# Performance work log

Hardware: AMD Instinct MI355X
Metric: run time of the kernel (lower is better)

## Reference

```python
import jax, jax.numpy as jnp
import numpy as np

L, N, C, OPL = 20, 512, 10, 13        # levels, nodes/level, conditions/node, condition op length
HID, MID = 512, 256                   # hidden_dim, hid_dim
OP_DIM, EX_DIM, SAMP_DIM = 15, 108, 1000
EPS = 1e-5


def _lstm_cell(x, h, c, wih, whh, bih, bhh):
    gates = x @ wih.T + h @ whh.T + bih + bhh
    i, f, g, o = jnp.split(gates, 4, axis=-1)  # torch gate order i,f,g,o
    c = jax.nn.sigmoid(f) * c + jax.nn.sigmoid(i) * jnp.tanh(g)
    h = jax.nn.sigmoid(o) * jnp.tanh(c)
    return h, c


def _batchnorm(x, g, b):  # training-mode BatchNorm1d (biased batch stats)
    m = x.mean(0)
    v = x.var(0)
    return (x - m) / jnp.sqrt(v + EPS) * g + b


def setup_inputs() -> dict:
    key = jax.random.key(0)
    ks = iter(jax.random.split(key, 48))
    rn = lambda shp, s=1.0: jax.random.normal(next(ks), shp, jnp.float32) * s
    ru = lambda shp: jax.random.uniform(next(ks), shp, jnp.float32)
    w = lambda shp: rn(shp, 0.05)
    inp = {
        'operators': ru((L, N, OP_DIM)),
        'extra_infos': rn((L, N, EX_DIM)),
        'condition1s': rn((L, N, C, OPL)),
        'condition2s': rn((L, N, C, OPL)),
        'samples': ru((L, N, SAMP_DIM)),
        'condition_masks': jnp.ones((L, N, 1), jnp.float32),
        'mapping': jax.random.randint(next(ks), (L, 2, N), 0, N + 1),
        # lstm1 (condition encoder)
        'w_ih1': w((4 * HID, OPL)), 'w_hh1': w((4 * HID, HID)),
        'b_ih1': w((4 * HID,)), 'b_hh1': w((4 * HID,)),
        # mlps feeding the tree lstm
        'sample_w': w((MID, SAMP_DIM)), 'sample_b': w((MID,)),
        'cond_w': w((MID, HID)), 'cond_b': w((MID,)),
        'bn1_g': jnp.ones((MID,), jnp.float32), 'bn1_b': jnp.zeros((MID,), jnp.float32),
        # lstm2 (tree aggregation)
        'w_ih2': w((4 * HID, OP_DIM + EX_DIM + 2 * MID)), 'w_hh2': w((4 * HID, HID)),
        'b_ih2': w((4 * HID,)), 'b_hh2': w((4 * HID,)),
        'bn2_g': jnp.ones((HID,), jnp.float32), 'bn2_b': jnp.zeros((HID,), jnp.float32),
        # task heads
        't1_w2': w((MID, HID)), 't1_b2': w((MID,)),
        't2_w2': w((MID, HID)), 't2_b2': w((MID,)),
        'bn3_g': jnp.ones((MID,), jnp.float32), 'bn3_b': jnp.zeros((MID,), jnp.float32),
        't1_w3': w((MID, MID)), 't1_b3': w((MID,)),
        't2_w3': w((MID, MID)), 't2_b3': w((MID,)),
        't1_ow': w((1, MID)), 't1_ob': w((1,)),
        't2_ow': w((1, MID)), 't2_ob': w((1,)),
    }
    return inp


def reference(operators, extra_infos, condition1s, condition2s, samples, condition_masks, mapping,
              w_ih1, w_hh1, b_ih1, b_hh1, sample_w, sample_b, cond_w, cond_b, bn1_g, bn1_b,
              w_ih2, w_hh2, b_ih2, b_hh2, bn2_g, bn2_b,
              t1_w2, t1_b2, t2_w2, t2_b2, bn3_g, bn3_b,
              t1_w3, t1_b3, t2_w3, t2_b3, t1_ow, t1_ob, t2_ow, t2_ob):
    Lv, Np = operators.shape[0], operators.shape[1]
    mapping = mapping.astype(jnp.int32)

    # --- condition encoder: lstm1 over each node's predicate sequence ---
    x = condition1s.reshape(Lv * Np, C, OPL)
    h0 = jnp.zeros((Lv * Np, HID), operators.dtype)

    def step1(carry, xt):
        h, c = carry
        h, c = _lstm_cell(xt, h, c, w_ih1, w_hh1, b_ih1, b_hh1)
        return (h, c), None

    (h_last, _), _ = jax.lax.scan(step1, (h0, h0), jnp.swapaxes(x, 0, 1))
    cond = _batchnorm(jax.nn.relu(h_last @ cond_w.T + cond_b), bn1_g, bn1_b)
    cond = cond.reshape(Lv, Np, MID)

    samp = jax.nn.relu(samples @ sample_w.T + sample_b) * condition_masks
    feats = jnp.concatenate([operators, extra_infos, cond, samp], axis=2)  # [L, N, 123+2*MID]

    # --- bottom level: lstm2 single step from zero state ---
    z0 = jnp.zeros((Np, HID), feats.dtype)
    hid, cid = _lstm_cell(feats[Lv - 1], z0, z0, w_ih2, w_hh2, b_ih2, b_hh2)

    # --- bottom-up tree aggregation: gather children states, average, lstm2 step ---
    def level_step(carry, inputs):
        hid, cid = carry
        x_lvl, mapp = inputs  # x_lvl [N, F], mapp [2, N], index 0 == pad (no child)
        pad = jnp.zeros((1, HID), hid.dtype)
        nh = jnp.concatenate([pad, hid], axis=0)  # [N+1, H]
        nc = jnp.concatenate([pad, cid], axis=0)
        h = (nh[mapp[0]] + nh[mapp[1]]) * 0.5
        c = (nc[mapp[0]] + nc[mapp[1]]) * 0.5
        hid, cid = _lstm_cell(x_lvl, h, c, w_ih2, w_hh2, b_ih2, b_hh2)
        return (hid, cid), None

    xs = (feats[Lv - 2::-1], mapping[Lv - 2::-1])
    (hid, cid), _ = jax.lax.scan(level_step, (hid, cid), xs)

    # --- heads (batch_size == Np: all level-0 nodes active for these inputs) ---
    z = _batchnorm(hid, bn2_g, bn2_b)
    t1 = _batchnorm(jax.nn.relu(z @ t1_w2.T + t1_b2), bn3_g, bn3_b)
    t1 = jax.nn.sigmoid(jax.nn.relu(t1 @ t1_w3.T + t1_b3) @ t1_ow.T + t1_ob)
    t2 = _batchnorm(jax.nn.relu(z @ t2_w2.T + t2_b2), bn3_g, bn3_b)
    t2 = jax.nn.sigmoid(jax.nn.relu(t2 @ t2_w3.T + t2_b3) @ t2_ow.T + t2_ob)
    return t1, t2
```

## Files before the change

kernel.cpp:

```cpp
#include <hip/hip_runtime.h>
#include <hip/hip_bf16.h>


typedef __bf16 bf16x8 __attribute__((ext_vector_type(8)));
typedef float f32x4 __attribute__((ext_vector_type(4)));

#define MROWS 10240
#define LDH1  552
#define L1_ROWS 48
#define L1_BLOCKS 214

#define PF_BIAS1   0
#define PF_BIAS2   2048
#define PF_CONDB   4096
#define PF_SAMPB   4352
#define PF_BCAT2   4608
#define PF_B3CAT   5120
#define PF_BN1G    5632
#define PF_BN1B    5888
#define PF_BN2G    6144
#define PF_BN2B    6656
#define PF_BN3G    7168
#define PF_BN3B    7424
#define PF_OW      7680
#define PF_OB      8192
#define PF_TOTAL   8194

__device__ __forceinline__ float fsig(float x) {
  return __builtin_amdgcn_rcpf(1.0f + __expf(-x));
}
__device__ __forceinline__ float ftanh(float x) {
  return fmaf(2.0f, __builtin_amdgcn_rcpf(1.0f + __expf(-2.0f * x)), -1.0f);
}
__device__ __forceinline__ bf16x8 bzero8() {
  bf16x8 z;
#pragma unroll
  for (int i = 0; i < 8; ++i) z[i] = (__bf16)0.0f;
  return z;
}
__device__ __forceinline__ float ld_in(const void* p, long i, int bf) {
  return bf ? (float)((const __bf16*)p)[i] : ((const float*)p)[i];
}

__global__ void detect_kernel(const unsigned* __restrict__ masks, int* __restrict__ flag) {
  if (blockIdx.x == 0 && threadIdx.x == 0)
    *flag = (masks[0] == 0x3F803F80u) ? 1 : 0;
}

__global__ void prep_kernel(const int* __restrict__ flagp,
    const void* w_ih1, const void* w_hh1, const void* b_ih1, const void* b_hh1,
    const void* w_ih2, const void* w_hh2, const void* b_ih2, const void* b_hh2,
    const void* t1_w2, const void* t2_w2, const void* t1_b2, const void* t2_b2,
    const void* cond_w, const void* cond_b, const void* sample_w, const void* sample_b,
    const void* bn1_g, const void* bn1_b, const void* bn2_g, const void* bn2_b,
    const void* bn3_g, const void* bn3_b,
    const void* t1_w3, const void* t1_b3, const void* t2_w3, const void* t2_b3,
    const void* t1_ow, const void* t1_ob, const void* t2_ow, const void* t2_ob,
    const void* masks,
    __bf16* __restrict__ w1s, __bf16* __restrict__ w2s,
    __bf16* __restrict__ wcat2, __bf16* __restrict__ cond_w_bf,
    __bf16* __restrict__ sample_w_bf, __bf16* __restrict__ w3cat_bf,
    float* __restrict__ mask_f, float* __restrict__ pf)
{
  const int bf = *flagp;
  const int S1 = 2048 * 544;
  const int S2 = 2048 * 1152;
  const int S3 = 512 * 512;
  const int S4 = 256 * 512;
  const int S5 = 256 * 1000;
  const int S6 = 512 * 256;
  const int S7 = 10240;
  const int total = S1 + S2 + S3 + S4 + S5 + S6 + S7 + PF_TOTAL;
  for (int idx = blockIdx.x * blockDim.x + threadIdx.x; idx < total;
       idx += gridDim.x * blockDim.x) {
    int i = idx;
    if (i < S1) {
      int e = i & 7, l = (i >> 3) & 63, g = (i >> 9) & 3;
      int grp = i >> 11;
      int kk = grp % 17, cgt = grp / 17;
      int colq = l & 15, quad = l >> 4;
      int row = g * 512 + cgt * 16 + colq;
      int k = kk * 32 + quad * 8 + e;
      float v = (k < 512) ? ld_in(w_hh1, (long)row * 512 + k, bf)
              : (k < 525) ? ld_in(w_ih1, (long)row * 13 + (k - 512), bf) : 0.0f;
      w1s[i] = (__bf16)v;
      continue;
    }
    i -= S1;
    if (i < S2) {
      int e = i & 7, l = (i >> 3) & 63, g = (i >> 9) & 3;
      int grp = i >> 11;
      int kk = grp % 36, jt = grp / 36;
      int colq = l & 15, quad = l >> 4;
      int row = g * 512 + jt * 16 + colq;
      int k = kk * 32 + quad * 8 + e;
      float v = (k < 635) ? ld_in(w_ih2, (long)row * 635 + k, bf)
              : (k < 640) ? 0.0f : ld_in(w_hh2, (long)row * 512 + (k - 640), bf);
      w2s[i] = (__bf16)v;
      continue;
    }
    i -= S2;
    if (i < S3) {
      int r = i >> 9, k = i & 511;
      wcat2[i] = (__bf16)((r < 256) ? ld_in(t1_w2, r * 512 + k, bf)
                                    : ld_in(t2_w2, (r - 256) * 512 + k, bf));
      continue;
    }
    i -= S3;
    if (i < S4) { cond_w_bf[i] = (__bf16)ld_in(cond_w, i, bf); continue; }
    i -= S4;
    if (i < S5) { sample_w_bf[i] = (__bf16)ld_in(sample_w, i, bf); continue; }
    i -= S5;
    if (i < S6) {
      int r = i >> 8, k = i & 255;
      w3cat_bf[i] = (__bf16)((r < 256) ? ld_in(t1_w3, r * 256 + k, bf)
                                       : ld_in(t2_w3, (r - 256) * 256 + k, bf));
      continue;
    }
    i -= S6;
    if (i < S7) { mask_f[i] = ld_in(masks, i, bf); continue; }
    i -= S7;
    {
      int j = i;
      float v;
      if      (j < 2048) v = ld_in(b_ih1, j, bf) + ld_in(b_hh1, j, bf);
      else if (j < 4096) v = ld_in(b_ih2, j - 2048, bf) + ld_in(b_hh2, j - 2048, bf);
      else if (j < 4352) v = ld_in(cond_b, j - 4096, bf);
      else if (j < 4608) v = ld_in(sample_b, j - 4352, bf);
      else if (j < 5120) { int k = j - 4608; v = (k < 256) ? ld_in(t1_b2, k, bf) : ld_in(t2_b2, k - 256, bf); }
      else if (j < 5632) { int k = j - 5120; v = (k < 256) ? ld_in(t1_b3, k, bf) : ld_in(t2_b3, k - 256, bf); }
      else if (j < 5888) v = ld_in(bn1_g, j - 5632, bf);
      else if (j < 6144) v = ld_in(bn1_b, j - 5888, bf);
      else if (j < 6656) v = ld_in(bn2_g, j - 6144, bf);
      else if (j < 7168) v = ld_in(bn2_b, j - 6656, bf);
      else if (j < 7424) v = ld_in(bn3_g, j - 7168, bf);
      else if (j < 7680) v = ld_in(bn3_b, j - 7424, bf);
      else if (j < 8192) { int k = j - 7680; v = (k < 256) ? ld_in(t1_ow, k, bf) : ld_in(t2_ow, k - 256, bf); }
      else v = (j == 8192) ? ld_in(t1_ob, 0, bf) : ld_in(t2_ob, 0, bf);
      pf[j] = v;
    }
  }
}

__global__ void conv_samples_kernel(const int* __restrict__ flagp,
                                    const void* __restrict__ samples,
                                    __bf16* __restrict__ dst)
{
  const int bf = *flagp;
  if (bf) return;
  for (long i = blockIdx.x * blockDim.x + threadIdx.x; i < 10240000L;
       i += (long)gridDim.x * blockDim.x)
    dst[i] = (__bf16)ld_in(samples, i, bf);
}

__global__ void featcopy_kernel(const int* __restrict__ flagp,
                                const void* __restrict__ ops,
                                const void* __restrict__ extra,
                                __bf16* __restrict__ Astage)
{
  const int bf = *flagp;
  int idx = blockIdx.x * blockDim.x + threadIdx.x;
  int m = idx >> 7, c = idx & 127;
  float v; int col;
  if (c < 15)       { v = ld_in(ops, (long)m * 15 + c, bf);            col = c; }
  else if (c < 123) { v = ld_in(extra, (long)m * 108 + (c - 15), bf);  col = c; }
  else              { v = 0.0f;                                        col = 512 + c; }
  Astage[(size_t)m * 640 + col] = (__bf16)v;
}

__global__ __launch_bounds__(1024, 4) void lstm1_kernel(
    const int* __restrict__ flagp,
    const void* __restrict__ cond1,
    const __bf16* __restrict__ w1s,
    const float*  __restrict__ bias,
    __bf16* __restrict__ h_out)
{
  __shared__ __attribute__((aligned(16))) __bf16 hbuf[2][L1_ROWS * LDH1];
  const int bf   = *flagp;
  const int tid  = threadIdx.x;
  const int wave = tid >> 6;
  const int lane = tid & 63;
  const int colq = lane & 15;
  const int quad = lane >> 4;
  const int r0   = blockIdx.x * L1_ROWS;

  {
    bf16x8 z8 = bzero8();
    for (int i = tid * 8; i < 2 * L1_ROWS * LDH1; i += 1024 * 8)
      *(bf16x8*)&hbuf[0][i] = z8;
  }
  __syncthreads();
  if (tid < L1_ROWS * 8) {
    int row = tid >> 3, jj = tid & 7;
    int gr = r0 + row;
    if (gr < MROWS) {
      long base = (long)gr * 130;
      hbuf[0][row * LDH1 + 512 + jj] = (__bf16)ld_in(cond1, base + jj, bf);
      if (jj < 5) hbuf[0][row * LDH1 + 520 + jj] = (__bf16)ld_in(cond1, base + 8 + jj, bf);
    }
  }
  __syncthreads();

  float c_reg[2][3][4];
#pragma unroll
  for (int a = 0; a < 2; ++a)
#pragma unroll
    for (int b = 0; b < 3; ++b)
#pragma unroll
      for (int r = 0; r < 4; ++r) c_reg[a][b][r] = 0.0f;

  const int jbase = wave * 32;

  float bI[2], bF[2], bG[2], bO[2];
#pragma unroll
  for (int cg = 0; cg < 2; ++cg) {
    const int j = jbase + cg * 16 + colq;
    bI[cg] = bias[j];
    bF[cg] = bias[512 + j];
    bG[cg] = bias[1024 + j];
    bO[cg] = bias[1536 + j];
  }

#pragma unroll 1
  for (int t = 0; t < 10; ++t) {
    const __bf16* hcur = hbuf[t & 1];
    __bf16* hnxt = hbuf[(t + 1) & 1];
#pragma unroll
    for (int cg = 0; cg < 2; ++cg) {
      const int jc = jbase + cg * 16;
      f32x4 acc[3][4];
#pragma unroll
      for (int a = 0; a < 3; ++a)
#pragma unroll
        for (int g = 0; g < 4; ++g)
#pragma unroll
          for (int r = 0; r < 4; ++r) acc[a][g][r] = 0.0f;

      const __bf16* wp = w1s + ((size_t)(wave * 2 + cg) * 17 * 4 * 512) + (lane << 3);
#pragma unroll 1
      for (int kk = 0; kk < 17; ++kk) {
        const int kof = (kk << 5) + (quad << 3);
        bf16x8 af[3];
#pragma unroll
        for (int rt = 0; rt < 3; ++rt)
          af[rt] = *(const bf16x8*)&hcur[(rt * 16 + colq) * LDH1 + kof];
        bf16x8 bfr[4];
#pragma unroll
        for (int g = 0; g < 4; ++g)
          bfr[g] = *(const bf16x8*)&wp[(kk * 4 + g) << 9];
#pragma unroll
        for (int g = 0; g < 4; ++g)
#pragma unroll
          for (int rt = 0; rt < 3; ++rt)
            acc[rt][g] = __builtin_amdgcn_mfma_f32_16x16x32_bf16(af[rt], bfr[g], acc[rt][g], 0, 0, 0);
      }
#pragma unroll
      for (int rt = 0; rt < 3; ++rt)
#pragma unroll
        for (int r = 0; r < 4; ++r) {
          float c = fsig(acc[rt][1][r] + bF[cg]) * c_reg[cg][rt][r]
                  + fsig(acc[rt][0][r] + bI[cg]) * ftanh(acc[rt][2][r] + bG[cg]);
          c_reg[cg][rt][r] = c;
          float h = fsig(acc[rt][3][r] + bO[cg]) * ftanh(c);
          hnxt[(rt * 16 + quad * 4 + r) * LDH1 + jc + colq] = (__bf16)h;
        }
    }
    if (t < 9 && tid < L1_ROWS * 8) {
      int row = tid >> 3, jj = tid & 7;
      int gr = r0 + row;
      if (gr < MROWS) {
        long base = ((long)gr * 10 + (t + 1)) * 13;
        hnxt[row * LDH1 + 512 + jj] = (__bf16)ld_in(cond1, base + jj, bf);
        if (jj < 5) hnxt[row * LDH1 + 520 + jj] = (__bf16)ld_in(cond1, base + 8 + jj, bf);
      }
    }
    __syncthreads();
  }

  for (int i = tid; i < L1_ROWS * 64; i += 1024) {
    int row = i >> 6;
    int cb  = (i & 63) << 3;
    *(bf16x8*)&h_out[(size_t)(r0 + row) * 512 + cb] = *(const bf16x8*)&hbuf[0][row * LDH1 + cb];
  }
}

template<int ACT, int OUTBF, int MASKED>
__global__ __launch_bounds__(256, 4) void gemm_kernel(
    const __bf16* __restrict__ A, int lda,
    const __bf16* __restrict__ W, int ldw,
    const float* __restrict__ bias,
    float* __restrict__ outf, __bf16* __restrict__ outb, int ldc,
    const float* __restrict__ mask, int K)
{
  const int tid  = threadIdx.x;
  const int wave = tid >> 6;
  const int lane = tid & 63;
  const int colq = lane & 15;
  const int quad = lane >> 4;
  const int m0 = blockIdx.y * 64 + (wave >> 1) * 32;
  const int n0 = blockIdx.x * 64 + (wave & 1) * 32;

  f32x4 acc[2][2];
#pragma unroll
  for (int a = 0; a < 2; ++a)
#pragma unroll
    for (int b = 0; b < 2; ++b)
#pragma unroll
      for (int r = 0; r < 4; ++r) acc[a][b][r] = 0.0f;

  const int nk = (K + 31) >> 5;
  for (int kk = 0; kk < nk; ++kk) {
    const int kof = (kk << 5) + (quad << 3);
    bf16x8 a0, a1, b0, b1;
    if (kof < K) {
      a0 = *(const bf16x8*)&A[(size_t)(m0 + colq) * lda + kof];
      a1 = *(const bf16x8*)&A[(size_t)(m0 + 16 + colq) * lda + kof];
      b0 = *(const bf16x8*)&W[(size_t)(n0 + colq) * ldw + kof];
      b1 = *(const bf16x8*)&W[(size_t)(n0 + 16 + colq) * ldw + kof];
    } else {
      a0 = bzero8(); a1 = a0; b0 = a0; b1 = a0;
    }
    acc[0][0] = __builtin_amdgcn_mfma_f32_16x16x32_bf16(a0, b0, acc[0][0], 0, 0, 0);
    acc[0][1] = __builtin_amdgcn_mfma_f32_16x16x32_bf16(a0, b1, acc[0][1], 0, 0, 0);
    acc[1][0] = __builtin_amdgcn_mfma_f32_16x16x32_bf16(a1, b0, acc[1][0], 0, 0, 0);
    acc[1][1] = __builtin_amdgcn_mfma_f32_16x16x32_bf16(a1, b1, acc[1][1], 0, 0, 0);
  }
#pragma unroll
  for (int ai = 0; ai < 2; ++ai)
#pragma unroll
    for (int bi = 0; bi < 2; ++bi) {
      const int col = n0 + bi * 16 + colq;
      const float bv = bias[col];
#pragma unroll
      for (int r = 0; r < 4; ++r) {
        const int row = m0 + ai * 16 + quad * 4 + r;
        float v = acc[ai][bi][r] + bv;
        if (ACT) v = fmaxf(v, 0.0f);
        if (MASKED) v *= mask[row];
        if (OUTBF) outb[(size_t)row * ldc + col] = (__bf16)v;
        else       outf[(size_t)row * ldc + col] = v;
      }
    }
}

__global__ __launch_bounds__(256, 4) void sampgemm_kernel(
    const int* __restrict__ flagp,
    const void* __restrict__ samples_raw,
    const __bf16* __restrict__ samp_bf,
    const __bf16* __restrict__ W,
    const float* __restrict__ bias,
    __bf16* __restrict__ outb,
    const float* __restrict__ mask)
{
  const __bf16* A = (*flagp) ? (const __bf16*)samples_raw : samp_bf;
  const int tid  = threadIdx.x;
  const int wave = tid >> 6;
  const int lane = tid & 63;
  const int colq = lane & 15;
  const int quad = lane >> 4;
  const int m0 = blockIdx.y * 64 + (wave >> 1) * 32;
  const int n0 = blockIdx.x * 64 + (wave & 1) * 32;
  const int K = 1000;

  f32x4 acc[2][2];
#pragma unroll
  for (int a = 0; a < 2; ++a)
#pragma unroll
    for (int b = 0; b < 2; ++b)
#pragma unroll
      for (int r = 0; r < 4; ++r) acc[a][b][r] = 0.0f;

  for (int kk = 0; kk < 32; ++kk) {
    const int kof = (kk << 5) + (quad << 3);
    bf16x8 a0, a1, b0, b1;
    if (kof < K) {
      a0 = *(const bf16x8*)&A[(size_t)(m0 + colq) * 1000 + kof];
      a1 = *(const bf16x8*)&A[(size_t)(m0 + 16 + colq) * 1000 + kof];
      b0 = *(const bf16x8*)&W[(size_t)(n0 + colq) * 1000 + kof];
      b1 = *(const bf16x8*)&W[(size_t)(n0 + 16 + colq) * 1000 + kof];
    } else {
      a0 = bzero8(); a1 = a0; b0 = a0; b1 = a0;
    }
    acc[0][0] = __builtin_amdgcn_mfma_f32_16x16x32_bf16(a0, b0, acc[0][0], 0, 0, 0);
    acc[0][1] = __builtin_amdgcn_mfma_f32_16x16x32_bf16(a0, b1, acc[0][1], 0, 0, 0);
    acc[1][0] = __builtin_amdgcn_mfma_f32_16x16x32_bf16(a1, b0, acc[1][0], 0, 0, 0);
    acc[1][1] = __builtin_amdgcn_mfma_f32_16x16x32_bf16(a1, b1, acc[1][1], 0, 0, 0);
  }
#pragma unroll
  for (int ai = 0; ai < 2; ++ai)
#pragma unroll
    for (int bi = 0; bi < 2; ++bi) {
      const int col = n0 + bi * 16 + colq;
      const float bv = bias[col];
#pragma unroll
      for (int r = 0; r < 4; ++r) {
        const int row = m0 + ai * 16 + quad * 4 + r;
        float v = fmaxf(acc[ai][bi][r] + bv, 0.0f) * mask[row];
        outb[(size_t)row * 640 + col] = (__bf16)v;
      }
    }
}

__global__ __launch_bounds__(1024, 4) void treelvl_kernel(
    const __bf16* __restrict__ Alvl,
    const __bf16* __restrict__ w2s,
    const float* __restrict__ bias,
    const int* __restrict__ mapping,
    const __bf16* __restrict__ h_src, const float* __restrict__ c_src,
    __bf16* __restrict__ h_dst, float* __restrict__ c_dst,
    float* __restrict__ h_f32, int first, int last)
{
  __shared__ float red[3][16 * 256];
  const int tid  = threadIdx.x;
  const int wave = tid >> 6;
  const int lane = tid & 63;
  const int colq = lane & 15;
  const int quad = lane >> 4;
  const int wv   = wave & 3;
  const int kq   = wave >> 2;
  const int jt = blockIdx.x;
  const int mt = blockIdx.y;
  const int rowA = mt * 64 + wv * 16 + colq;

  const __bf16* wbase = w2s + (size_t)jt * 36 * 4 * 512 + (lane << 3);

  f32x4 acc[4];
#pragma unroll
  for (int g = 0; g < 4; ++g)
#pragma unroll
    for (int r = 0; r < 4; ++r) acc[g][r] = 0.0f;

  if (kq < 2) {
    const __bf16* arow = Alvl + (size_t)rowA * 640;
    const int kb = kq * 10;
#pragma unroll 2
    for (int ki = 0; ki < 10; ++ki) {
      const int kk = kb + ki;
      const int kof = (kk << 5) + (quad << 3);
      bf16x8 afr = *(const bf16x8*)&arow[kof];
      bf16x8 b0 = *(const bf16x8*)&wbase[(kk * 4 + 0) << 9];
      bf16x8 b1 = *(const bf16x8*)&wbase[(kk * 4 + 1) << 9];
      bf16x8 b2 = *(const bf16x8*)&wbase[(kk * 4 + 2) << 9];
      bf16x8 b3 = *(const bf16x8*)&wbase[(kk * 4 + 3) << 9];
      acc[0] = __builtin_amdgcn_mfma_f32_16x16x32_bf16(afr, b0, acc[0], 0, 0, 0);
      acc[1] = __builtin_amdgcn_mfma_f32_16x16x32_bf16(afr, b1, acc[1], 0, 0, 0);
      acc[2] = __builtin_amdgcn_mfma_f32_16x16x32_bf16(afr, b2, acc[2], 0, 0, 0);
      acc[3] = __builtin_amdgcn_mfma_f32_16x16x32_bf16(afr, b3, acc[3], 0, 0, 0);
    }
  } else {
    int i0 = 0, i1 = 0;
    if (!first) { i0 = mapping[rowA]; i1 = mapping[512 + rowA]; }
    const float s0 = (i0 > 0) ? 0.5f : 0.0f;
    const float s1 = (i1 > 0) ? 0.5f : 0.0f;
    const __bf16* h0p = h_src + (size_t)((i0 > 0 ? i0 : 1) - 1) * 512;
    const __bf16* h1p = h_src + (size_t)((i1 > 0 ? i1 : 1) - 1) * 512;
    const int kb = 20 + (kq - 2) * 8;
#pragma unroll 2
    for (int ki = 0; ki < 8; ++ki) {
      const int kk = kb + ki;
      const int kh = ((kk - 20) << 5) + (quad << 3);
      bf16x8 v0 = *(const bf16x8*)&h0p[kh];
      bf16x8 v1 = *(const bf16x8*)&h1p[kh];
      bf16x8 afr;
#pragma unroll
      for (int e = 0; e < 8; ++e)
        afr[e] = (__bf16)((float)v0[e] * s0 + (float)v1[e] * s1);
      bf16x8 b0 = *(const bf16x8*)&wbase[(kk * 4 + 0) << 9];
      bf16x8 b1 = *(const bf16x8*)&wbase[(kk * 4 + 1) << 9];
      bf16x8 b2 = *(const bf16x8*)&wbase[(kk * 4 + 2) << 9];
      bf16x8 b3 = *(const bf16x8*)&wbase[(kk * 4 + 3) << 9];
      acc[0] = __builtin_amdgcn_mfma_f32_16x16x32_bf16(afr, b0, acc[0], 0, 0, 0);
      acc[1] = __builtin_amdgcn_mfma_f32_16x16x32_bf16(afr, b1, acc[1], 0, 0, 0);
      acc[2] = __builtin_amdgcn_mfma_f32_16x16x32_bf16(afr, b2, acc[2], 0, 0, 0);
      acc[3] = __builtin_amdgcn_mfma_f32_16x16x32_bf16(afr, b3, acc[3], 0, 0, 0);
    }
  }

  if (kq > 0) {
    float* rp = red[kq - 1];
    const int base = wv * 64 + lane;
#pragma unroll
    for (int g = 0; g < 4; ++g)
#pragma unroll
      for (int r = 0; r < 4; ++r)
        rp[(g * 4 + r) * 256 + base] = acc[g][r];
  }
  __syncthreads();
  if (kq != 0) return;

  {
    const int base = wv * 64 + lane;
#pragma unroll
    for (int s = 0; s < 3; ++s) {
      const float* rp = red[s];
#pragma unroll
      for (int g = 0; g < 4; ++g)
#pragma unroll
        for (int r = 0; r < 4; ++r)
          acc[g][r] += rp[(g * 4 + r) * 256 + base];
    }
  }

  const int j = jt * 16 + colq;
  const float bi  = bias[j];
  const float bff = bias[512 + j];
  const float bg  = bias[1024 + j];
  const float bo  = bias[1536 + j];
#pragma unroll
  for (int r = 0; r < 4; ++r) {
    const int mrow = mt * 64 + wv * 16 + quad * 4 + r;
    float ci = 0.0f;
    if (!first) {
      int a0 = mapping[mrow], a1 = mapping[512 + mrow];
      if (a0 > 0) ci += c_src[(size_t)(a0 - 1) * 512 + j];
      if (a1 > 0) ci += c_src[(size_t)(a1 - 1) * 512 + j];
      ci *= 0.5f;
    }
    float c = fsig(acc[1][r] + bff) * ci + fsig(acc[0][r] + bi) * ftanh(acc[2][r] + bg);
    float h = fsig(acc[3][r] + bo) * ftanh(c);
    h_dst[(size_t)mrow * 512 + j] = (__bf16)h;
    c_dst[(size_t)mrow * 512 + j] = c;
    if (last) h_f32[(size_t)mrow * 512 + j] = h;
  }
}

__global__ void stats1_kernel(const float* __restrict__ in, int ld, int N,
                              int rows_per_blk, float* __restrict__ partial)
{
  int b = blockIdx.x;
  int r0 = b * rows_per_blk;
  for (int c = threadIdx.x; c < N; c += blockDim.x) {
    float s = 0.0f, sq = 0.0f;
    for (int r = 0; r < rows_per_blk; ++r) {
      float v = in[(size_t)(r0 + r) * ld + c];
      s += v; sq += v * v;
    }
    partial[(size_t)(2 * b) * N + c] = s;
    partial[(size_t)(2 * b + 1) * N + c] = sq;
  }
}

__global__ void stats2_kernel(const float* __restrict__ partial, int nb, int N,
                              float invM, float* __restrict__ stats)
{
  int c = blockIdx.x * blockDim.x + threadIdx.x;
  if (c >= N) return;
  float s = 0.0f, sq = 0.0f;
  for (int b = 0; b < nb; ++b) {
    s  += partial[(size_t)(2 * b) * N + c];
    sq += partial[(size_t)(2 * b + 1) * N + c];
  }
  float mean = s * invM;
  float var  = sq * invM - mean * mean;
  stats[c]     = mean;
  stats[N + c] = rsqrtf(fmaxf(var, 0.0f) + 1e-5f);
}

__global__ void norm_kernel(const float* __restrict__ in, int ldin,
                            const float* __restrict__ stats, int N, int cshift, int gmask,
                            const float* __restrict__ g, const float* __restrict__ b,
                            __bf16* __restrict__ outp, int ldc, int total)
{
  for (int idx = blockIdx.x * blockDim.x + threadIdx.x; idx < total;
       idx += gridDim.x * blockDim.x) {
    int row = idx >> cshift;
    int c = idx & (N - 1);
    float v = (in[(size_t)row * ldin + c] - stats[c]) * stats[N + c];
    int gi = c & gmask;
    v = v * g[gi] + b[gi];
    outp[(size_t)row * ldc + c] = (__bf16)v;
  }
}

__global__ void head_kernel(const int* __restrict__ flagp,
                            const __bf16* __restrict__ tmp3,
                            const float* __restrict__ pf,
                            void* __restrict__ outp)
{
  const int bf = *flagp;
  const int gw   = blockIdx.x * 4 + (threadIdx.x >> 6);
  const int lane = threadIdx.x & 63;
  const int which = gw >> 9;
  const int n     = gw & 511;
  const __bf16* row = tmp3 + (size_t)n * 512 + which * 256;
  const float* ow = pf + PF_OW + which * 256;
  float s = 0.0f;
#pragma unroll
  for (int i = 0; i < 4; ++i) {
    const int k = lane + 64 * i;
    s += (float)row[k] * ow[k];
  }
#pragma unroll
  for (int off = 32; off > 0; off >>= 1)
    s += __shfl_down(s, off);
  if (lane == 0) {
    float v = fsig(s + pf[PF_OB + which]);
    if (bf) ((__bf16*)outp)[gw] = (__bf16)v;
    else    ((float*)outp)[gw]  = v;
  }
}

extern "C" void kernel_launch(void* const* d_in, const int* in_sizes, int n_in,
                              void* d_out, int out_size, void* d_ws, size_t ws_size,
                              hipStream_t stream) {
  const void* operators       = d_in[0];
  const void* extra_infos     = d_in[1];
  const void* condition1s     = d_in[2];
  const void* samples         = d_in[4];
  const void* condition_masks = d_in[5];
  const int*  mapping         = (const int*)d_in[6];
  (void)in_sizes; (void)n_in; (void)out_size; (void)ws_size;

  char* ws = (char*)d_ws;
  size_t off = 0;
  auto alloc = [&](size_t bytes) -> void* {
    void* p = ws + off;
    off += (bytes + 255) & ~(size_t)255;
    return p;
  };
  int*    flag     = (int*)   alloc(256);
  __bf16* w1s      = (__bf16*)alloc((size_t)2048 * 544 * 2);
  __bf16* w2s      = (__bf16*)alloc((size_t)2048 * 1152 * 2);
  __bf16* wcat2    = (__bf16*)alloc(512 * 512 * 2);
  __bf16* cond_w_bf   = (__bf16*)alloc(256 * 512 * 2);
  __bf16* sample_w_bf = (__bf16*)alloc(256 * 1000 * 2);
  __bf16* w3cat_bf    = (__bf16*)alloc(512 * 256 * 2);
  float*  mask_f   = (float*) alloc(10240 * 4);
  float*  pf       = (float*) alloc(PF_TOTAL * 4);
  __bf16* samp_bf  = (__bf16*)alloc((size_t)10240 * 1000 * 2);
  __bf16* h_last   = (__bf16*)alloc((size_t)10272 * 512 * 2);
  float*  condtmp  = (float*) alloc((size_t)10240 * 256 * 4);
  __bf16* Astage   = (__bf16*)alloc((size_t)20 * 512 * 640 * 2);
  __bf16* hs0      = (__bf16*)alloc(512 * 512 * 2);
  __bf16* hs1      = (__bf16*)alloc(512 * 512 * 2);
  float*  cs0      = (float*) alloc(512 * 512 * 4);
  float*  cs1      = (float*) alloc(512 * 512 * 4);
  float*  h_f32    = (float*) alloc(512 * 512 * 4);
  __bf16* zbuf     = (__bf16*)alloc(512 * 512 * 2);
  float*  tmp1     = (float*) alloc(512 * 512 * 4);
  __bf16* tmp2     = (__bf16*)alloc(512 * 512 * 2);
  __bf16* tmp3     = (__bf16*)alloc(512 * 512 * 2);
  float*  partial  = (float*) alloc(64 * 2 * 512 * 4);
  float*  statsb   = (float*) alloc(2 * 512 * 4);

  detect_kernel<<<1, 64, 0, stream>>>((const unsigned*)condition_masks, flag);
  prep_kernel<<<4096, 256, 0, stream>>>(flag,
      d_in[7], d_in[8], d_in[9], d_in[10],
      d_in[17], d_in[18], d_in[19], d_in[20],
      d_in[23], d_in[25], d_in[24], d_in[26],
      d_in[13], d_in[14], d_in[11], d_in[12],
      d_in[15], d_in[16], d_in[21], d_in[22],
      d_in[27], d_in[28],
      d_in[29], d_in[30], d_in[31], d_in[32],
      d_in[33], d_in[34], d_in[35], d_in[36],
      condition_masks,
      w1s, w2s, wcat2, cond_w_bf, sample_w_bf, w3cat_bf, mask_f, pf);
  conv_samples_kernel<<<4096, 256, 0, stream>>>(flag, samples, samp_bf);
  featcopy_kernel<<<5120, 256, 0, stream>>>(flag, operators, extra_infos, Astage);
  lstm1_kernel<<<L1_BLOCKS, 1024, 0, stream>>>(flag, condition1s, w1s, pf + PF_BIAS1, h_last);

  gemm_kernel<1,0,0><<<dim3(4,160), 256, 0, stream>>>(h_last, 512, cond_w_bf, 512,
      pf + PF_CONDB, condtmp, nullptr, 256, nullptr, 512);
  stats1_kernel<<<64, 256, 0, stream>>>(condtmp, 256, 256, 160, partial);
  stats2_kernel<<<1, 256, 0, stream>>>(partial, 64, 256, 1.0f / 10240.0f, statsb);
  norm_kernel<<<2560, 256, 0, stream>>>(condtmp, 256, statsb, 256, 8, 255,
      pf + PF_BN1G, pf + PF_BN1B, Astage + 123, 640, 10240 * 256);

  sampgemm_kernel<<<dim3(4,160), 256, 0, stream>>>(flag, samples, samp_bf,
      sample_w_bf, pf + PF_SAMPB, Astage + 379, mask_f);

  for (int lvl = 19; lvl >= 0; --lvl) {
    __bf16* hd = (lvl & 1) ? hs1 : hs0;
    float*  cd = (lvl & 1) ? cs1 : cs0;
    const __bf16* hsrc = (lvl & 1) ? hs0 : hs1;
    const float*  csrc = (lvl & 1) ? cs0 : cs1;
    treelvl_kernel<<<dim3(32,8), 1024, 0, stream>>>(
        Astage + (size_t)lvl * 512 * 640, w2s, pf + PF_BIAS2,
        mapping + lvl * 1024, hsrc, csrc, hd, cd, h_f32,
        (lvl == 19) ? 1 : 0, (lvl == 0) ? 1 : 0);
  }

  stats1_kernel<<<8, 256, 0, stream>>>(h_f32, 512, 512, 64, partial);
  stats2_kernel<<<2, 256, 0, stream>>>(partial, 8, 512, 1.0f / 512.0f, statsb);
  norm_kernel<<<256, 256, 0, stream>>>(h_f32, 512, statsb, 512, 9, 511,
      pf + PF_BN2G, pf + PF_BN2B, zbuf, 512, 512 * 512);

  gemm_kernel<1,0,0><<<dim3(8,8), 256, 0, stream>>>(zbuf, 512, wcat2, 512,
      pf + PF_BCAT2, tmp1, nullptr, 512, nullptr, 512);
  stats1_kernel<<<8, 256, 0, stream>>>(tmp1, 512, 512, 64, partial);
  stats2_kernel<<<2, 256, 0, stream>>>(partial, 8, 512, 1.0f / 512.0f, statsb);
  norm_kernel<<<256, 256, 0, stream>>>(tmp1, 512, statsb, 512, 9, 255,
      pf + PF_BN3G, pf + PF_BN3B, tmp2, 512, 512 * 512);

  gemm_kernel<1,1,0><<<dim3(4,8), 256, 0, stream>>>(tmp2, 512, w3cat_bf, 256,
      pf + PF_B3CAT, nullptr, tmp3, 512, nullptr, 256);
  gemm_kernel<1,1,0><<<dim3(4,8), 256, 0, stream>>>(tmp2 + 256, 512, w3cat_bf + 256 * 256, 256,
      pf + PF_B3CAT + 256, nullptr, tmp3 + 256, 512, nullptr, 256);

  head_kernel<<<256, 256, 0, stream>>>(flag, tmp3, pf, d_out);
}
```

Before: 955.3 us.

## Fuse lstm1, sample GEMM and feature copy into one heterogeneous launch

Merges the condition LSTM kernel, the sample MLP GEMM and the operator/extra feature copy into a single kernel, dispatching by block index. Blocks below 214 run the LSTM, the next 160 blocks each run four 256-thread GEMM tiles, and the last 40 blocks run a grid-stride feature copy. The aim is to overlap the independent sample GEMM and copy with the long-running LSTM blocks and to save launches. The GEMM and copy branches now run under 1024-thread blocks sized for the LSTM's shared memory and launch bounds, which may lower their occupancy.

```diff
diff --git a/kernel.cpp b/kernel.cpp
--- a/kernel.cpp
+++ b/kernel.cpp
@@ -9,6 +9,9 @@
 #define LDH1  552
 #define L1_ROWS 48
 #define L1_BLOCKS 214
+#define SAMP_BASE 214
+#define FEAT_BASE 374
+#define FUSED_BLOCKS 414
 
 #define PF_BIAS1   0
 #define PF_BIAS2   2048
@@ -153,134 +156,196 @@
     dst[i] = (__bf16)ld_in(samples, i, bf);
 }
 
-__global__ void featcopy_kernel(const int* __restrict__ flagp,
-                                const void* __restrict__ ops,
-                                const void* __restrict__ extra,
-                                __bf16* __restrict__ Astage)
-{
-  const int bf = *flagp;
-  int idx = blockIdx.x * blockDim.x + threadIdx.x;
-  int m = idx >> 7, c = idx & 127;
-  float v; int col;
-  if (c < 15)       { v = ld_in(ops, (long)m * 15 + c, bf);            col = c; }
-  else if (c < 123) { v = ld_in(extra, (long)m * 108 + (c - 15), bf);  col = c; }
-  else              { v = 0.0f;                                        col = 512 + c; }
-  Astage[(size_t)m * 640 + col] = (__bf16)v;
-}
-
-__global__ __launch_bounds__(1024, 4) void lstm1_kernel(
+__global__ __launch_bounds__(1024, 4) void fused1_kernel(
     const int* __restrict__ flagp,
     const void* __restrict__ cond1,
     const __bf16* __restrict__ w1s,
     const float*  __restrict__ bias,
-    __bf16* __restrict__ h_out)
-{
-  __shared__ __attribute__((aligned(16))) __bf16 hbuf[2][L1_ROWS * LDH1];
-  const int bf   = *flagp;
-  const int tid  = threadIdx.x;
-  const int wave = tid >> 6;
-  const int lane = tid & 63;
-  const int colq = lane & 15;
-  const int quad = lane >> 4;
-  const int r0   = blockIdx.x * L1_ROWS;
-
-  {
-    bf16x8 z8 = bzero8();
-    for (int i = tid * 8; i < 2 * L1_ROWS * LDH1; i += 1024 * 8)
-      *(bf16x8*)&hbuf[0][i] = z8;
-  }
-  __syncthreads();
-  if (tid < L1_ROWS * 8) {
-    int row = tid >> 3, jj = tid & 7;
-    int gr = r0 + row;
-    if (gr < MROWS) {
-      long base = (long)gr * 130;
-      hbuf[0][row * LDH1 + 512 + jj] = (__bf16)ld_in(cond1, base + jj, bf);
-      if (jj < 5) hbuf[0][row * LDH1 + 520 + jj] = (__bf16)ld_in(cond1, base + 8 + jj, bf);
-    }
-  }
-  __syncthreads();
-
-  float c_reg[2][3][4];
-#pragma unroll
-  for (int a = 0; a < 2; ++a)
-#pragma unroll
-    for (int b = 0; b < 3; ++b)
-#pragma unroll
-      for (int r = 0; r < 4; ++r) c_reg[a][b][r] = 0.0f;
-
-  const int jbase = wave * 32;
-
-  float bI[2], bF[2], bG[2], bO[2];
-#pragma unroll
-  for (int cg = 0; cg < 2; ++cg) {
-    const int j = jbase + cg * 16 + colq;
-    bI[cg] = bias[j];
-    bF[cg] = bias[512 + j];
-    bG[cg] = bias[1024 + j];
-    bO[cg] = bias[1536 + j];
-  }
-
-#pragma unroll 1
-  for (int t = 0; t < 10; ++t) {
-    const __bf16* hcur = hbuf[t & 1];
-    __bf16* hnxt = hbuf[(t + 1) & 1];
-#pragma unroll
-    for (int cg = 0; cg < 2; ++cg) {
-      const int jc = jbase + cg * 16;
-      f32x4 acc[3][4];
-#pragma unroll
-      for (int a = 0; a < 3; ++a)
-#pragma unroll
-        for (int g = 0; g < 4; ++g)
-#pragma unroll
-          for (int r = 0; r < 4; ++r) acc[a][g][r] = 0.0f;
-
-      const __bf16* wp = w1s + ((size_t)(wave * 2 + cg) * 17 * 4 * 512) + (lane << 3);
-#pragma unroll 1
-      for (int kk = 0; kk < 17; ++kk) {
-        const int kof = (kk << 5) + (quad << 3);
-        bf16x8 af[3];
-#pragma unroll
-        for (int rt = 0; rt < 3; ++rt)
-          af[rt] = *(const bf16x8*)&hcur[(rt * 16 + colq) * LDH1 + kof];
-        bf16x8 bfr[4];
-#pragma unroll
-        for (int g = 0; g < 4; ++g)
-          bfr[g] = *(const bf16x8*)&wp[(kk * 4 + g) << 9];
-#pragma unroll
-        for (int g = 0; g < 4; ++g)
-#pragma unroll
-          for (int rt = 0; rt < 3; ++rt)
-            acc[rt][g] = __builtin_amdgcn_mfma_f32_16x16x32_bf16(af[rt], bfr[g], acc[rt][g], 0, 0, 0);
-      }
-#pragma unroll
-      for (int rt = 0; rt < 3; ++rt)
-#pragma unroll
-        for (int r = 0; r < 4; ++r) {
-          float c = fsig(acc[rt][1][r] + bF[cg]) * c_reg[cg][rt][r]
-                  + fsig(acc[rt][0][r] + bI[cg]) * ftanh(acc[rt][2][r] + bG[cg]);
-          c_reg[cg][rt][r] = c;
-          float h = fsig(acc[rt][3][r] + bO[cg]) * ftanh(c);
-          hnxt[(rt * 16 + quad * 4 + r) * LDH1 + jc + colq] = (__bf16)h;
-        }
-    }
-    if (t < 9 && tid < L1_ROWS * 8) {
+    __bf16* __restrict__ h_out,
+    const void* __restrict__ samples_raw,
+    const __bf16* __restrict__ samp_bf,
+    const __bf16* __restrict__ sample_w_bf,
+    const float* __restrict__ sampb,
+    __bf16* __restrict__ samp_out,
+    const float* __restrict__ mask,
+    const void* __restrict__ ops,
+    const void* __restrict__ extra,
+    __bf16* __restrict__ Astage)
+{
+  const int bf = *flagp;
+  const int tid = threadIdx.x;
+
+  if (blockIdx.x < L1_BLOCKS) {
+    __shared__ __attribute__((aligned(16))) __bf16 hbuf[2][L1_ROWS * LDH1];
+    const int wave = tid >> 6;
+    const int lane = tid & 63;
+    const int colq = lane & 15;
+    const int quad = lane >> 4;
+    const int r0   = blockIdx.x * L1_ROWS;
+
+    {
+      bf16x8 z8 = bzero8();
+      for (int i = tid * 8; i < 2 * L1_ROWS * LDH1; i += 1024 * 8)
+        *(bf16x8*)&hbuf[0][i] = z8;
+    }
+    __syncthreads();
+    if (tid < L1_ROWS * 8) {
       int row = tid >> 3, jj = tid & 7;
       int gr = r0 + row;
       if (gr < MROWS) {
-        long base = ((long)gr * 10 + (t + 1)) * 13;
-        hnxt[row * LDH1 + 512 + jj] = (__bf16)ld_in(cond1, base + jj, bf);
-        if (jj < 5) hnxt[row * LDH1 + 520 + jj] = (__bf16)ld_in(cond1, base + 8 + jj, bf);
+        long base = (long)gr * 130;
+        hbuf[0][row * LDH1 + 512 + jj] = (__bf16)ld_in(cond1, base + jj, bf);
+        if (jj < 5) hbuf[0][row * LDH1 + 520 + jj] = (__bf16)ld_in(cond1, base + 8 + jj, bf);
       }
     }
     __syncthreads();
-  }
-
-  for (int i = tid; i < L1_ROWS * 64; i += 1024) {
-    int row = i >> 6;
-    int cb  = (i & 63) << 3;
-    *(bf16x8*)&h_out[(size_t)(r0 + row) * 512 + cb] = *(const bf16x8*)&hbuf[0][row * LDH1 + cb];
+
+    float c_reg[2][3][4];
+#pragma unroll
+    for (int a = 0; a < 2; ++a)
+#pragma unroll
+      for (int b = 0; b < 3; ++b)
+#pragma unroll
+        for (int r = 0; r < 4; ++r) c_reg[a][b][r] = 0.0f;
+
+    const int jbase = wave * 32;
+
+    float bI[2], bF[2], bG[2], bO[2];
+#pragma unroll
+    for (int cg = 0; cg < 2; ++cg) {
+      const int j = jbase + cg * 16 + colq;
+      bI[cg] = bias[j];
+      bF[cg] = bias[512 + j];
+      bG[cg] = bias[1024 + j];
+      bO[cg] = bias[1536 + j];
+    }
+
+#pragma unroll 1
+    for (int t = 0; t < 10; ++t) {
+      const __bf16* hcur = hbuf[t & 1];
+      __bf16* hnxt = hbuf[(t + 1) & 1];
+#pragma unroll
+      for (int cg = 0; cg < 2; ++cg) {
+        const int jc = jbase + cg * 16;
+        f32x4 acc[3][4];
+#pragma unroll
+        for (int a = 0; a < 3; ++a)
+#pragma unroll
+          for (int g = 0; g < 4; ++g)
+#pragma unroll
+            for (int r = 0; r < 4; ++r) acc[a][g][r] = 0.0f;
+
+        const __bf16* wp = w1s + ((size_t)(wave * 2 + cg) * 17 * 4 * 512) + (lane << 3);
+#pragma unroll 1
+        for (int kk = 0; kk < 17; ++kk) {
+          const int kof = (kk << 5) + (quad << 3);
+          bf16x8 af[3];
+#pragma unroll
+          for (int rt = 0; rt < 3; ++rt)
+            af[rt] = *(const bf16x8*)&hcur[(rt * 16 + colq) * LDH1 + kof];
+          bf16x8 bfr[4];
+#pragma unroll
+          for (int g = 0; g < 4; ++g)
+            bfr[g] = *(const bf16x8*)&wp[(kk * 4 + g) << 9];
+#pragma unroll
+          for (int g = 0; g < 4; ++g)
+#pragma unroll
+            for (int rt = 0; rt < 3; ++rt)
+              acc[rt][g] = __builtin_amdgcn_mfma_f32_16x16x32_bf16(af[rt], bfr[g], acc[rt][g], 0, 0, 0);
+        }
+#pragma unroll
+        for (int rt = 0; rt < 3; ++rt)
+#pragma unroll
+          for (int r = 0; r < 4; ++r) {
+            float c = fsig(acc[rt][1][r] + bF[cg]) * c_reg[cg][rt][r]
+                    + fsig(acc[rt][0][r] + bI[cg]) * ftanh(acc[rt][2][r] + bG[cg]);
+            c_reg[cg][rt][r] = c;
+            float h = fsig(acc[rt][3][r] + bO[cg]) * ftanh(c);
+            hnxt[(rt * 16 + quad * 4 + r) * LDH1 + jc + colq] = (__bf16)h;
+          }
+      }
+      if (t < 9 && tid < L1_ROWS * 8) {
+        int row = tid >> 3, jj = tid & 7;
+        int gr = r0 + row;
+        if (gr < MROWS) {
+          long base = ((long)gr * 10 + (t + 1)) * 13;
+          hnxt[row * LDH1 + 512 + jj] = (__bf16)ld_in(cond1, base + jj, bf);
+          if (jj < 5) hnxt[row * LDH1 + 520 + jj] = (__bf16)ld_in(cond1, base + 8 + jj, bf);
+        }
+      }
+      __syncthreads();
+    }
+
+    for (int i = tid; i < L1_ROWS * 64; i += 1024) {
+      int row = i >> 6;
+      int cb  = (i & 63) << 3;
+      *(bf16x8*)&h_out[(size_t)(r0 + row) * 512 + cb] = *(const bf16x8*)&hbuf[0][row * LDH1 + cb];
+    }
+    return;
+  }
+
+  if (blockIdx.x < FEAT_BASE) {
+    const __bf16* A = bf ? (const __bf16*)samples_raw : samp_bf;
+    const int vb   = (blockIdx.x - SAMP_BASE) * 4 + (tid >> 8);
+    const int bx   = vb & 3;
+    const int by   = vb >> 2;
+    const int t    = tid & 255;
+    const int wave = t >> 6;
+    const int lane = t & 63;
+    const int colq = lane & 15;
+    const int quad = lane >> 4;
+    const int m0 = by * 64 + (wave >> 1) * 32;
+    const int n0 = bx * 64 + (wave & 1) * 32;
+    const int K = 1000;
+
+    f32x4 acc[2][2];
+#pragma unroll
+    for (int a = 0; a < 2; ++a)
+#pragma unroll
+      for (int b = 0; b < 2; ++b)
+#pragma unroll
+        for (int r = 0; r < 4; ++r) acc[a][b][r] = 0.0f;
+
+    for (int kk = 0; kk < 32; ++kk) {
+      const int kof = (kk << 5) + (quad << 3);
+      bf16x8 a0, a1, b0, b1;
+      if (kof < K) {
+        a0 = *(const bf16x8*)&A[(size_t)(m0 + colq) * 1000 + kof];
+        a1 = *(const bf16x8*)&A[(size_t)(m0 + 16 + colq) * 1000 + kof];
+        b0 = *(const bf16x8*)&sample_w_bf[(size_t)(n0 + colq) * 1000 + kof];
+        b1 = *(const bf16x8*)&sample_w_bf[(size_t)(n0 + 16 + colq) * 1000 + kof];
+      } else {
+        a0 = bzero8(); a1 = a0; b0 = a0; b1 = a0;
+      }
+      acc[0][0] = __builtin_amdgcn_mfma_f32_16x16x32_bf16(a0, b0, acc[0][0], 0, 0, 0);
+      acc[0][1] = __builtin_amdgcn_mfma_f32_16x16x32_bf16(a0, b1, acc[0][1], 0, 0, 0);
+      acc[1][0] = __builtin_amdgcn_mfma_f32_16x16x32_bf16(a1, b0, acc[1][0], 0, 0, 0);
+      acc[1][1] = __builtin_amdgcn_mfma_f32_16x16x32_bf16(a1, b1, acc[1][1], 0, 0, 0);
+    }
+#pragma unroll
+    for (int ai = 0; ai < 2; ++ai)
+#pragma unroll
+      for (int bi = 0; bi < 2; ++bi) {
+        const int col = n0 + bi * 16 + colq;
+        const float bv = sampb[col];
+#pragma unroll
+        for (int r = 0; r < 4; ++r) {
+          const int row = m0 + ai * 16 + quad * 4 + r;
+          float v = fmaxf(acc[ai][bi][r] + bv, 0.0f) * mask[row];
+          samp_out[(size_t)row * 640 + col] = (__bf16)v;
+        }
+      }
+    return;
+  }
+
+  for (int idx = (blockIdx.x - FEAT_BASE) * 1024 + tid; idx < 10240 * 128;
+       idx += 40 * 1024) {
+    int m = idx >> 7, c = idx & 127;
+    float v; int col;
+    if (c < 15)       { v = ld_in(ops, (long)m * 15 + c, bf);            col = c; }
+    else if (c < 123) { v = ld_in(extra, (long)m * 108 + (c - 15), bf);  col = c; }
+    else              { v = 0.0f;                                        col = 512 + c; }
+    Astage[(size_t)m * 640 + col] = (__bf16)v;
   }
 }
 
@@ -339,64 +404,6 @@
         if (MASKED) v *= mask[row];
         if (OUTBF) outb[(size_t)row * ldc + col] = (__bf16)v;
         else       outf[(size_t)row * ldc + col] = v;
-      }
-    }
-}
-
-__global__ __launch_bounds__(256, 4) void sampgemm_kernel(
-    const int* __restrict__ flagp,
-    const void* __restrict__ samples_raw,
-    const __bf16* __restrict__ samp_bf,
-    const __bf16* __restrict__ W,
-    const float* __restrict__ bias,
-    __bf16* __restrict__ outb,
-    const float* __restrict__ mask)
-{
-  const __bf16* A = (*flagp) ? (const __bf16*)samples_raw : samp_bf;
-  const int tid  = threadIdx.x;
-  const int wave = tid >> 6;
-  const int lane = tid & 63;
-  const int colq = lane & 15;
-  const int quad = lane >> 4;
-  const int m0 = blockIdx.y * 64 + (wave >> 1) * 32;
-  const int n0 = blockIdx.x * 64 + (wave & 1) * 32;
-  const int K = 1000;
-
-  f32x4 acc[2][2];
-#pragma unroll
-  for (int a = 0; a < 2; ++a)
-#pragma unroll
-    for (int b = 0; b < 2; ++b)
-#pragma unroll
-      for (int r = 0; r < 4; ++r) acc[a][b][r] = 0.0f;
-
-  for (int kk = 0; kk < 32; ++kk) {
-    const int kof = (kk << 5) + (quad << 3);
-    bf16x8 a0, a1, b0, b1;
-    if (kof < K) {
-      a0 = *(const bf16x8*)&A[(size_t)(m0 + colq) * 1000 + kof];
-      a1 = *(const bf16x8*)&A[(size_t)(m0 + 16 + colq) * 1000 + kof];
-      b0 = *(const bf16x8*)&W[(size_t)(n0 + colq) * 1000 + kof];
-      b1 = *(const bf16x8*)&W[(size_t)(n0 + 16 + colq) * 1000 + kof];
-    } else {
-      a0 = bzero8(); a1 = a0; b0 = a0; b1 = a0;
-    }
-    acc[0][0] = __builtin_amdgcn_mfma_f32_16x16x32_bf16(a0, b0, acc[0][0], 0, 0, 0);
-    acc[0][1] = __builtin_amdgcn_mfma_f32_16x16x32_bf16(a0, b1, acc[0][1], 0, 0, 0);
-    acc[1][0] = __builtin_amdgcn_mfma_f32_16x16x32_bf16(a1, b0, acc[1][0], 0, 0, 0);
-    acc[1][1] = __builtin_amdgcn_mfma_f32_16x16x32_bf16(a1, b1, acc[1][1], 0, 0, 0);
-  }
-#pragma unroll
-  for (int ai = 0; ai < 2; ++ai)
-#pragma unroll
-    for (int bi = 0; bi < 2; ++bi) {
-      const int col = n0 + bi * 16 + colq;
-      const float bv = bias[col];
-#pragma unroll
-      for (int r = 0; r < 4; ++r) {
-        const int row = m0 + ai * 16 + quad * 4 + r;
-        float v = fmaxf(acc[ai][bi][r] + bv, 0.0f) * mask[row];
-        outb[(size_t)row * 640 + col] = (__bf16)v;
       }
     }
 }
@@ -655,9 +662,13 @@
       d_in[33], d_in[34], d_in[35], d_in[36],
       condition_masks,
       w1s, w2s, wcat2, cond_w_bf, sample_w_bf, w3cat_bf, mask_f, pf);
+
   conv_samples_kernel<<<4096, 256, 0, stream>>>(flag, samples, samp_bf);
-  featcopy_kernel<<<5120, 256, 0, stream>>>(flag, operators, extra_infos, Astage);
-  lstm1_kernel<<<L1_BLOCKS, 1024, 0, stream>>>(flag, condition1s, w1s, pf + PF_BIAS1, h_last);
+
+  fused1_kernel<<<FUSED_BLOCKS, 1024, 0, stream>>>(flag,
+      condition1s, w1s, pf + PF_BIAS1, h_last,
+      samples, samp_bf, sample_w_bf, pf + PF_SAMPB, Astage + 379, mask_f,
+      operators, extra_infos, Astage);
 
   gemm_kernel<1,0,0><<<dim3(4,160), 256, 0, stream>>>(h_last, 512, cond_w_bf, 512,
       pf + PF_CONDB, condtmp, nullptr, 256, nullptr, 512);
@@ -665,9 +676,6 @@
   stats2_kernel<<<1, 256, 0, stream>>>(partial, 64, 256, 1.0f / 10240.0f, statsb);
   norm_kernel<<<2560, 256, 0, stream>>>(condtmp, 256, statsb, 256, 8, 255,
       pf + PF_BN1G, pf + PF_BN1B, Astage + 123, 640, 10240 * 256);
-
-  sampgemm_kernel<<<dim3(4,160), 256, 0, stream>>>(flag, samples, samp_bf,
-      sample_w_bf, pf + PF_SAMPB, Astage + 379, mask_f);
 
   for (int lvl = 19; lvl >= 0; --lvl) {
     __bf16* hd = (lvl & 1) ? hs1 : hs0;
```

Measured after the change: 934.6 us. -2.2%, faster.
